# Performance work log

Hardware: AMD Instinct MI355X
Metric: run time of the kernel (lower is better)

Reference implementation:

```python
import jax, jax.numpy as jnp
import numpy as np

B, S_REF, E, H = 128, 2048, 512, 512

def setup_inputs() -> dict:
    key = jax.random.key(0)
    ks = jax.random.split(key, 13)
    def lin(kw, kb, out_d, in_d):
        bound = 1.0 / np.sqrt(in_d)
        w = jax.random.uniform(kw, (out_d, in_d), minval=-bound, maxval=bound, dtype=jnp.float32)
        b = jax.random.uniform(kb, (out_d,), minval=-bound, maxval=bound, dtype=jnp.float32)
        return w, b
    Wa_w, Wa_b = lin(ks[0], ks[1], H, H)
    Ua_w, Ua_b = lin(ks[2], ks[3], H, H)
    Va_w, Va_b = lin(ks[4], ks[5], 1, H)
    Wih_w, Wih_b = lin(ks[6], ks[7], H, E + H)
    Whh_w, Whh_b = lin(ks[8], ks[9], H, H)
    x_t = jax.random.normal(ks[10], (B, 1, E), dtype=jnp.float32)
    x_ref_encoded = jax.random.normal(ks[11], (B, S_REF, H), dtype=jnp.float32)
    h_prev = jax.random.normal(ks[12], (B, H), dtype=jnp.float32)
    return {"x_t": x_t, "x_ref_encoded": x_ref_encoded, "h_prev": h_prev,
            "Wa_w": Wa_w, "Wa_b": Wa_b, "Ua_w": Ua_w, "Ua_b": Ua_b,
            "Va_w": Va_w, "Va_b": Va_b, "Wih_w": Wih_w, "Wih_b": Wih_b,
            "Whh_w": Whh_w, "Whh_b": Whh_b}

def reference(x_t, x_ref_encoded, h_prev, Wa_w, Wa_b, Ua_w, Ua_b, Va_w, Va_b, Wih_w, Wih_b, Whh_w, Whh_b):
    # Bahdanau additive attention
    q = h_prev @ Wa_w.T + Wa_b                      # (B, H)
    k = jnp.einsum('bsh,oh->bso', x_ref_encoded, Ua_w) + Ua_b  # (B, S, H)
    scores = jnp.einsum('bsh,h->bs', jnp.tanh(q[:, None, :] + k), Va_w[0]) + Va_b[0]  # (B, S)
    attn_weights = jax.nn.softmax(scores, axis=1)
    context = jnp.einsum('bs,bsh->bh', attn_weights, x_ref_encoded)  # (B, H)
    # Reservoir RNN cell on concat(x_t[:,0,:], context)
    rnn_in = jnp.concatenate([x_t[:, 0, :], context], axis=1)        # (B, E+H)
    h_next = jnp.tanh(rnn_in @ Wih_w.T + Wih_b + h_prev @ Whh_w.T + Whh_b)
    return (h_next, context)
```

## Files before the change

kernel.cpp:

```cpp
#include <hip/hip_runtime.h>
#include <hip/hip_bf16.h>
#include <math.h>


typedef __attribute__((ext_vector_type(8))) short short8;
typedef __attribute__((ext_vector_type(8))) unsigned short ushort8;
typedef __attribute__((ext_vector_type(4))) float f32x4;

#define S_LEN 2048
#define BDIM 128
#define HDIM 512
#define EDIM 512
#define BM 64
#define NCHUNK (S_LEN / BM)

__device__ __forceinline__ unsigned short f2bf(float f) {
  unsigned int u = __float_as_uint(f);
  u += 0x7fffu + ((u >> 16) & 1u);
  return (unsigned short)(u >> 16);
}

__device__ __forceinline__ float bf2f(unsigned short u) {
  return __uint_as_float(((unsigned int)u) << 16);
}

__device__ __forceinline__ float fast_tanh(float x) {
  float e = __expf(2.0f * x);
  return 1.0f - 2.0f / (e + 1.0f);
}

__global__ __launch_bounds__(256) void k_prep(const float* __restrict__ ua_src,
                                              unsigned short* __restrict__ ua_dst,
                                              const float* __restrict__ hp,
                                              const float* __restrict__ Wa,
                                              const float* __restrict__ Wab,
                                              const float* __restrict__ Uab,
                                              float* __restrict__ q) {
  if (blockIdx.x < 128) {
    int tid = blockIdx.x * 256 + threadIdx.x;
    int ct = tid >> 10;
    int kt = (tid >> 6) & 15;
    int l = tid & 63;
    int col = ct * 16 + (l & 15);
    int k = kt * 32 + (l >> 4) * 8;
    const float4* s = (const float4*)(ua_src + (size_t)col * HDIM + k);
    float4 v0 = s[0], v1 = s[1];
    ushort8 p;
    p[0] = f2bf(v0.x); p[1] = f2bf(v0.y); p[2] = f2bf(v0.z); p[3] = f2bf(v0.w);
    p[4] = f2bf(v1.x); p[5] = f2bf(v1.y); p[6] = f2bf(v1.z); p[7] = f2bf(v1.w);
    *(ushort8*)(ua_dst + (size_t)tid * 8) = p;
  } else {
    int bq = blockIdx.x - 128;
    int b = bq >> 1, oh = bq & 1;
    int o = oh * 256 + threadIdx.x;
    __shared__ float hs[HDIM];
    hs[threadIdx.x] = hp[b * HDIM + threadIdx.x];
    hs[threadIdx.x + 256] = hp[b * HDIM + threadIdx.x + 256];
    __syncthreads();
    const float4* wr = (const float4*)(Wa + (size_t)o * HDIM);
    float acc = 0.f;
#pragma unroll 8
    for (int i = 0; i < HDIM / 4; ++i) {
      float4 v = wr[i];
      acc += v.x * hs[i * 4 + 0] + v.y * hs[i * 4 + 1] + v.z * hs[i * 4 + 2] + v.w * hs[i * 4 + 3];
    }
    q[b * HDIM + o] = acc + Wab[o] + Uab[o];
  }
}

__global__ __launch_bounds__(512, 4) void k_scores_ctx(
    const float* __restrict__ xref, const unsigned short* __restrict__ uab,
    const float* __restrict__ q, const float* __restrict__ va,
    float* __restrict__ mArr, float* __restrict__ lArr, float* __restrict__ cpart) {
  int chunk = blockIdx.x;
  int b = blockIdx.y;
  int tid = threadIdx.x;
  int l = tid & 63;
  int w = tid >> 6;
  int c = l & 15, g4 = l >> 4;

  __shared__ __align__(16) unsigned short As[BM * HDIM];
  __shared__ float sc[BM];
  __shared__ float pl[BM];

  f32x4 acc[4][4];
#pragma unroll
  for (int m = 0; m < 4; ++m)
#pragma unroll
    for (int n = 0; n < 4; ++n) acc[m][n] = f32x4{0.f, 0.f, 0.f, 0.f};

  const float* xb = xref + ((size_t)b * S_LEN + (size_t)chunk * BM) * HDIM;

  int srow = tid >> 3, skq = tid & 7;
  char* wb = (char*)&As[0] + srow * 1024 + ((skq * 16) ^ ((srow & 7) << 4));
  const float* sb = xb + (size_t)srow * HDIM + skq * 8;

  float4 a0, a1, a2, a3, a4, a5, a6, a7;
  short8 bpre[4];

#define LD2(va, vb, p)                                                         \
  {                                                                            \
    va = *(const float4*)(sb + (p) * 64);                                      \
    vb = *(const float4*)(sb + (p) * 64 + 4);                                  \
  }

#define WR1(va, vb, p)                                                         \
  {                                                                            \
    union { __hip_bfloat162 h[4]; ushort8 s; } u_;                             \
    u_.h[0] = __float22bfloat162_rn(make_float2(va.x, va.y));                  \
    u_.h[1] = __float22bfloat162_rn(make_float2(va.z, va.w));                  \
    u_.h[2] = __float22bfloat162_rn(make_float2(vb.x, vb.y));                  \
    u_.h[3] = __float22bfloat162_rn(make_float2(vb.z, vb.w));                  \
    *(ushort8*)(wb + (p) * 128) = u_.s;                                        \
  }

#define AFRAGS(kt)                                                             \
    short8 afr_[4];                                                            \
    _Pragma("unroll")                                                          \
    for (int m = 0; m < 4; ++m) {                                              \
      int row = m * 16 + (l & 15);                                             \
      int kb = ((kt) * 64 + (l >> 4) * 16) ^ ((row & 7) << 4);                 \
      afr_[m] = *(const short8*)((const char*)&As[0] + row * 1024 + kb);       \
    }

#define MFMA16(bsrc)                                                           \
    __builtin_amdgcn_s_setprio(1);                                             \
    _Pragma("unroll")                                                          \
    for (int m = 0; m < 4; ++m)                                                \
      _Pragma("unroll")                                                        \
      for (int n = 0; n < 4; ++n)                                              \
        acc[m][n] = __builtin_amdgcn_mfma_f32_16x16x32_bf16(afr_[m], bsrc[n],  \
                                                            acc[m][n], 0, 0, 0); \
    __builtin_amdgcn_s_setprio(0);

#define CLUSTER(kt)                                                            \
  {                                                                            \
    short8 bfr_[4];                                                            \
    _Pragma("unroll")                                                          \
    for (int n = 0; n < 4; ++n) {                                              \
      int ct = w * 4 + n;                                                      \
      bfr_[n] = *(const short8*)(uab + (((size_t)(ct * 16 + (kt)) * 64 + l) * 8)); \
    }                                                                          \
    AFRAGS(kt)                                                                 \
    MFMA16(bfr_)                                                               \
  }

#define CLUSTER_PRE(kt)                                                        \
  {                                                                            \
    AFRAGS(kt)                                                                 \
    MFMA16(bpre)                                                               \
  }

  LD2(a0, a1, 0) LD2(a2, a3, 1) LD2(a4, a5, 2) LD2(a6, a7, 3)
  WR1(a0, a1, 0) WR1(a2, a3, 1) WR1(a4, a5, 2) WR1(a6, a7, 3)
  LD2(a0, a1, 4) LD2(a2, a3, 5) LD2(a4, a5, 6) LD2(a6, a7, 7)
  WR1(a0, a1, 4) WR1(a2, a3, 5) WR1(a4, a5, 6) WR1(a6, a7, 7)
  if (tid < BM) sc[tid] = 0.f;
#pragma unroll
  for (int n = 0; n < 4; ++n)
    bpre[n] = *(const short8*)(uab + (((size_t)((w * 4 + n) * 16 + 0) * 64 + l) * 8));
  __syncthreads();

  CLUSTER_PRE(0)
  CLUSTER(1)  CLUSTER(2)  CLUSTER(3)
  CLUSTER(4)  CLUSTER(5)  CLUSTER(6)  CLUSTER(7)
  CLUSTER(8)  CLUSTER(9)  CLUSTER(10) CLUSTER(11)
  CLUSTER(12) CLUSTER(13)

  float qf[4], vf[4];
#pragma unroll
  for (int n = 0; n < 4; ++n) {
    int o = w * 64 + n * 16 + c;
    qf[n] = q[b * HDIM + o];
    vf[n] = va[o];
  }
  CLUSTER(14) CLUSTER(15)

#pragma unroll
  for (int m = 0; m < 4; ++m) {
#pragma unroll
    for (int r = 0; r < 4; ++r) {
      float sum = 0.f;
#pragma unroll
      for (int n = 0; n < 4; ++n) sum += fast_tanh(acc[m][n][r] + qf[n]) * vf[n];
      sum += __shfl_xor(sum, 1);
      sum += __shfl_xor(sum, 2);
      sum += __shfl_xor(sum, 4);
      sum += __shfl_xor(sum, 8);
      if (c == 0) atomicAdd(&sc[m * 16 + g4 * 4 + r], sum);
    }
  }
  __syncthreads();

  float M = sc[l];
#pragma unroll
  for (int off = 32; off >= 1; off >>= 1) M = fmaxf(M, __shfl_xor(M, off));
  float pp = __expf(sc[l] - M);
  float lsum = pp;
#pragma unroll
  for (int off = 32; off >= 1; off >>= 1) lsum += __shfl_xor(lsum, off);
  if (tid < BM) pl[tid] = pp;
  if (tid == 0) {
    mArr[b * NCHUNK + chunk] = M;
    lArr[b * NCHUNK + chunk] = lsum;
  }
  __syncthreads();

  {
    int h2 = tid * 2;
    const char* base_ = (const char*)&As[0];
    float cacc = 0.f;
#pragma unroll 8
    for (int r = 0; r < BM; ++r) {
      int byte = r * 1024 + (h2 ^ ((r & 7) << 4));
      cacc += pl[r] * bf2f(*(const unsigned short*)(base_ + byte));
    }
    cpart[((size_t)b * NCHUNK + chunk) * HDIM + tid] = cacc;
  }
#undef LD2
#undef WR1
#undef AFRAGS
#undef MFMA16
#undef CLUSTER
#undef CLUSTER_PRE
}

__global__ __launch_bounds__(512) void k_combine(const float* __restrict__ mArr,
                                                 const float* __restrict__ lArr,
                                                 const float* __restrict__ cpart,
                                                 float* __restrict__ ctx,
                                                 float* __restrict__ out_ctx) {
  int b = blockIdx.x, t = threadIdx.x;
  __shared__ float wf[NCHUNK];
  __shared__ float dinv;
  if (t == 0) {
    float M = mArr[b * NCHUNK];
    for (int i = 1; i < NCHUNK; ++i) M = fmaxf(M, mArr[b * NCHUNK + i]);
    float den = 0.f;
    for (int i = 0; i < NCHUNK; ++i) {
      float f = __expf(mArr[b * NCHUNK + i] - M);
      wf[i] = f;
      den += f * lArr[b * NCHUNK + i];
    }
    dinv = 1.0f / den;
  }
  __syncthreads();
  float s = 0.f;
#pragma unroll
  for (int i = 0; i < NCHUNK; ++i) s += wf[i] * cpart[((size_t)b * NCHUNK + i) * HDIM + t];
  float c = s * dinv;
  ctx[b * HDIM + t] = c;
  out_ctx[b * HDIM + t] = c;
}

__global__ __launch_bounds__(256) void k_rnn(const float* __restrict__ xt,
                                             const float* __restrict__ ctx,
                                             const float* __restrict__ hp,
                                             const float* __restrict__ Wih,
                                             const float* __restrict__ Wihb,
                                             const float* __restrict__ Whh,
                                             const float* __restrict__ Whhb,
                                             float* __restrict__ hout) {
  int b = blockIdx.x, oh = blockIdx.y;
  int o = oh * 256 + threadIdx.x;
  __shared__ float xs[EDIM], cs[HDIM], hs[HDIM];
  xs[threadIdx.x] = xt[b * EDIM + threadIdx.x];
  xs[threadIdx.x + 256] = xt[b * EDIM + threadIdx.x + 256];
  cs[threadIdx.x] = ctx[b * HDIM + threadIdx.x];
  cs[threadIdx.x + 256] = ctx[b * HDIM + threadIdx.x + 256];
  hs[threadIdx.x] = hp[b * HDIM + threadIdx.x];
  hs[threadIdx.x + 256] = hp[b * HDIM + threadIdx.x + 256];
  __syncthreads();
  const float4* wi = (const float4*)(Wih + (size_t)o * (EDIM + HDIM));
  float acc = Wihb[o] + Whhb[o];
#pragma unroll 8
  for (int i = 0; i < EDIM / 4; ++i) {
    float4 v = wi[i];
    acc += v.x * xs[i * 4] + v.y * xs[i * 4 + 1] + v.z * xs[i * 4 + 2] + v.w * xs[i * 4 + 3];
  }
  const float4* wi2 = wi + EDIM / 4;
#pragma unroll 8
  for (int i = 0; i < HDIM / 4; ++i) {
    float4 v = wi2[i];
    acc += v.x * cs[i * 4] + v.y * cs[i * 4 + 1] + v.z * cs[i * 4 + 2] + v.w * cs[i * 4 + 3];
  }
  const float4* wh = (const float4*)(Whh + (size_t)o * HDIM);
#pragma unroll 8
  for (int i = 0; i < HDIM / 4; ++i) {
    float4 v = wh[i];
    acc += v.x * hs[i * 4] + v.y * hs[i * 4 + 1] + v.z * hs[i * 4 + 2] + v.w * hs[i * 4 + 3];
  }
  hout[b * HDIM + o] = tanhf(acc);
}

extern "C" void kernel_launch(void* const* d_in, const int* in_sizes, int n_in,
                              void* d_out, int out_size, void* d_ws, size_t ws_size,
                              hipStream_t stream) {
  const float* x_t    = (const float*)d_in[0];
  const float* x_ref  = (const float*)d_in[1];
  const float* h_prev = (const float*)d_in[2];
  const float* Wa_w   = (const float*)d_in[3];
  const float* Wa_b   = (const float*)d_in[4];
  const float* Ua_w   = (const float*)d_in[5];
  const float* Ua_b   = (const float*)d_in[6];
  const float* Va_w   = (const float*)d_in[7];
  const float* Wih_w  = (const float*)d_in[9];
  const float* Wih_b  = (const float*)d_in[10];
  const float* Whh_w  = (const float*)d_in[11];
  const float* Whh_b  = (const float*)d_in[12];

  char* ws = (char*)d_ws;
  unsigned short* ua_fr = (unsigned short*)ws;
  float* q     = (float*)(ws + 524288);
  float* mArr  = (float*)(ws + 786432);
  float* lArr  = (float*)(ws + 802816);
  float* cpart = (float*)(ws + 819200);
  float* ctx   = (float*)(ws + 9207808);

  float* h_out   = (float*)d_out;
  float* ctx_out = h_out + BDIM * HDIM;

  k_prep<<<dim3(384), dim3(256), 0, stream>>>(Ua_w, ua_fr, h_prev, Wa_w, Wa_b, Ua_b, q);
  k_scores_ctx<<<dim3(NCHUNK, BDIM), dim3(512), 0, stream>>>(x_ref, ua_fr, q, Va_w, mArr, lArr, cpart);
  k_combine<<<dim3(BDIM), dim3(512), 0, stream>>>(mArr, lArr, cpart, ctx, ctx_out);
  k_rnn<<<dim3(BDIM, 2), dim3(256), 0, stream>>>(x_t, ctx, h_prev, Wih_w, Wih_b, Whh_w, Whh_b, h_out);
}
```

Measured before the change: 288.8 us.

## Double sequence tile to 128 rows and split output columns into two halves

Doubles the per-block sequence chunk from 64 to 128 rows, so each block loads a 128x512 bf16 tile into shared memory. The output dimension is then processed in two passes of 256 columns, each wave doing 8x2 MFMA tiles and a fused tanh/score epilogue per pass. The aim is to halve the number of chunks and the combine-stage partials, and to reuse each B fragment across more rows. In exchange, shared memory per block doubles, occupancy is capped at 2 blocks per CU, and the setprio hints are removed.

```diff
diff --git a/kernel.cpp b/kernel.cpp
--- a/kernel.cpp
+++ b/kernel.cpp
@@ -11,7 +11,7 @@
 #define BDIM 128
 #define HDIM 512
 #define EDIM 512
-#define BM 64
+#define BM 128
 #define NCHUNK (S_LEN / BM)
 
 __device__ __forceinline__ unsigned short f2bf(float f) {
@@ -68,7 +68,7 @@
   }
 }
 
-__global__ __launch_bounds__(512, 4) void k_scores_ctx(
+__global__ __launch_bounds__(512, 2) void k_scores_ctx(
     const float* __restrict__ xref, const unsigned short* __restrict__ uab,
     const float* __restrict__ q, const float* __restrict__ va,
     float* __restrict__ mArr, float* __restrict__ lArr, float* __restrict__ cpart) {
@@ -83,62 +83,63 @@
   __shared__ float sc[BM];
   __shared__ float pl[BM];
 
-  f32x4 acc[4][4];
-#pragma unroll
-  for (int m = 0; m < 4; ++m)
-#pragma unroll
-    for (int n = 0; n < 4; ++n) acc[m][n] = f32x4{0.f, 0.f, 0.f, 0.f};
+  f32x4 acc[8][2];
+#pragma unroll
+  for (int m = 0; m < 8; ++m)
+#pragma unroll
+    for (int n = 0; n < 2; ++n) acc[m][n] = f32x4{0.f, 0.f, 0.f, 0.f};
 
   const float* xb = xref + ((size_t)b * S_LEN + (size_t)chunk * BM) * HDIM;
 
   int srow = tid >> 3, skq = tid & 7;
-  char* wb = (char*)&As[0] + srow * 1024 + ((skq * 16) ^ ((srow & 7) << 4));
-  const float* sb = xb + (size_t)srow * HDIM + skq * 8;
+  int swo = (skq * 16) ^ ((srow & 7) << 4);
+  char* wb0 = (char*)&As[0] + srow * 1024 + swo;
+  char* wb1 = (char*)&As[0] + (srow + 64) * 1024 + swo;
+  const float* sb0 = xb + (size_t)srow * HDIM + skq * 8;
+  const float* sb1 = sb0 + (size_t)64 * HDIM;
 
   float4 a0, a1, a2, a3, a4, a5, a6, a7;
-  short8 bpre[4];
-
-#define LD2(va, vb, p)                                                         \
-  {                                                                            \
-    va = *(const float4*)(sb + (p) * 64);                                      \
-    vb = *(const float4*)(sb + (p) * 64 + 4);                                  \
-  }
-
-#define WR1(va, vb, p)                                                         \
+  short8 bpre[2];
+
+#define LD2(va, vb, sb, p)                                                     \
+  {                                                                            \
+    va = *(const float4*)((sb) + (p) * 64);                                    \
+    vb = *(const float4*)((sb) + (p) * 64 + 4);                                \
+  }
+
+#define WR1(va, vb, wb, p)                                                     \
   {                                                                            \
     union { __hip_bfloat162 h[4]; ushort8 s; } u_;                             \
     u_.h[0] = __float22bfloat162_rn(make_float2(va.x, va.y));                  \
     u_.h[1] = __float22bfloat162_rn(make_float2(va.z, va.w));                  \
     u_.h[2] = __float22bfloat162_rn(make_float2(vb.x, vb.y));                  \
     u_.h[3] = __float22bfloat162_rn(make_float2(vb.z, vb.w));                  \
-    *(ushort8*)(wb + (p) * 128) = u_.s;                                        \
+    *(ushort8*)((wb) + (p) * 128) = u_.s;                                      \
   }
 
 #define AFRAGS(kt)                                                             \
-    short8 afr_[4];                                                            \
+    short8 afr_[8];                                                            \
     _Pragma("unroll")                                                          \
-    for (int m = 0; m < 4; ++m) {                                              \
+    for (int m = 0; m < 8; ++m) {                                              \
       int row = m * 16 + (l & 15);                                             \
       int kb = ((kt) * 64 + (l >> 4) * 16) ^ ((row & 7) << 4);                 \
       afr_[m] = *(const short8*)((const char*)&As[0] + row * 1024 + kb);       \
     }
 
 #define MFMA16(bsrc)                                                           \
-    __builtin_amdgcn_s_setprio(1);                                             \
     _Pragma("unroll")                                                          \
-    for (int m = 0; m < 4; ++m)                                                \
+    for (int m = 0; m < 8; ++m)                                                \
       _Pragma("unroll")                                                        \
-      for (int n = 0; n < 4; ++n)                                              \
+      for (int n = 0; n < 2; ++n)                                              \
         acc[m][n] = __builtin_amdgcn_mfma_f32_16x16x32_bf16(afr_[m], bsrc[n],  \
-                                                            acc[m][n], 0, 0, 0); \
-    __builtin_amdgcn_s_setprio(0);
-
-#define CLUSTER(kt)                                                            \
-  {                                                                            \
-    short8 bfr_[4];                                                            \
+                                                            acc[m][n], 0, 0, 0);
+
+#define CLUSTER(h, kt)                                                         \
+  {                                                                            \
+    short8 bfr_[2];                                                            \
     _Pragma("unroll")                                                          \
-    for (int n = 0; n < 4; ++n) {                                              \
-      int ct = w * 4 + n;                                                      \
+    for (int n = 0; n < 2; ++n) {                                              \
+      int ct = (h) * 16 + w * 2 + n;                                           \
       bfr_[n] = *(const short8*)(uab + (((size_t)(ct * 16 + (kt)) * 64 + l) * 8)); \
     }                                                                          \
     AFRAGS(kt)                                                                 \
@@ -151,55 +152,71 @@
     MFMA16(bpre)                                                               \
   }
 
-  LD2(a0, a1, 0) LD2(a2, a3, 1) LD2(a4, a5, 2) LD2(a6, a7, 3)
-  WR1(a0, a1, 0) WR1(a2, a3, 1) WR1(a4, a5, 2) WR1(a6, a7, 3)
-  LD2(a0, a1, 4) LD2(a2, a3, 5) LD2(a4, a5, 6) LD2(a6, a7, 7)
-  WR1(a0, a1, 4) WR1(a2, a3, 5) WR1(a4, a5, 6) WR1(a6, a7, 7)
+#define EPI(h)                                                                 \
+  {                                                                            \
+    float qf0, qf1, vf0, vf1;                                                  \
+    {                                                                          \
+      int o0 = (h) * 256 + w * 32 + c, o1 = o0 + 16;                           \
+      qf0 = q[b * HDIM + o0]; qf1 = q[b * HDIM + o1];                          \
+      vf0 = va[o0]; vf1 = va[o1];                                              \
+    }                                                                          \
+    _Pragma("unroll")                                                          \
+    for (int m = 0; m < 8; ++m) {                                              \
+      _Pragma("unroll")                                                        \
+      for (int r = 0; r < 4; ++r) {                                            \
+        float sum = fast_tanh(acc[m][0][r] + qf0) * vf0 +                      \
+                    fast_tanh(acc[m][1][r] + qf1) * vf1;                       \
+        sum += __shfl_xor(sum, 1);                                             \
+        sum += __shfl_xor(sum, 2);                                             \
+        sum += __shfl_xor(sum, 4);                                             \
+        sum += __shfl_xor(sum, 8);                                             \
+        if (c == 0) atomicAdd(&sc[m * 16 + g4 * 4 + r], sum);                  \
+      }                                                                        \
+    }                                                                          \
+  }
+
+  LD2(a0, a1, sb0, 0) LD2(a2, a3, sb0, 1) LD2(a4, a5, sb0, 2) LD2(a6, a7, sb0, 3)
+  WR1(a0, a1, wb0, 0) WR1(a2, a3, wb0, 1) WR1(a4, a5, wb0, 2) WR1(a6, a7, wb0, 3)
+  LD2(a0, a1, sb0, 4) LD2(a2, a3, sb0, 5) LD2(a4, a5, sb0, 6) LD2(a6, a7, sb0, 7)
+  WR1(a0, a1, wb0, 4) WR1(a2, a3, wb0, 5) WR1(a4, a5, wb0, 6) WR1(a6, a7, wb0, 7)
+  LD2(a0, a1, sb1, 0) LD2(a2, a3, sb1, 1) LD2(a4, a5, sb1, 2) LD2(a6, a7, sb1, 3)
+  WR1(a0, a1, wb1, 0) WR1(a2, a3, wb1, 1) WR1(a4, a5, wb1, 2) WR1(a6, a7, wb1, 3)
+  LD2(a0, a1, sb1, 4) LD2(a2, a3, sb1, 5) LD2(a4, a5, sb1, 6) LD2(a6, a7, sb1, 7)
+  WR1(a0, a1, wb1, 4) WR1(a2, a3, wb1, 5) WR1(a4, a5, wb1, 6) WR1(a6, a7, wb1, 7)
   if (tid < BM) sc[tid] = 0.f;
 #pragma unroll
-  for (int n = 0; n < 4; ++n)
-    bpre[n] = *(const short8*)(uab + (((size_t)((w * 4 + n) * 16 + 0) * 64 + l) * 8));
+  for (int n = 0; n < 2; ++n)
+    bpre[n] = *(const short8*)(uab + (((size_t)((w * 2 + n) * 16 + 0) * 64 + l) * 8));
   __syncthreads();
 
   CLUSTER_PRE(0)
-  CLUSTER(1)  CLUSTER(2)  CLUSTER(3)
-  CLUSTER(4)  CLUSTER(5)  CLUSTER(6)  CLUSTER(7)
-  CLUSTER(8)  CLUSTER(9)  CLUSTER(10) CLUSTER(11)
-  CLUSTER(12) CLUSTER(13)
-
-  float qf[4], vf[4];
-#pragma unroll
-  for (int n = 0; n < 4; ++n) {
-    int o = w * 64 + n * 16 + c;
-    qf[n] = q[b * HDIM + o];
-    vf[n] = va[o];
-  }
-  CLUSTER(14) CLUSTER(15)
-
-#pragma unroll
-  for (int m = 0; m < 4; ++m) {
-#pragma unroll
-    for (int r = 0; r < 4; ++r) {
-      float sum = 0.f;
-#pragma unroll
-      for (int n = 0; n < 4; ++n) sum += fast_tanh(acc[m][n][r] + qf[n]) * vf[n];
-      sum += __shfl_xor(sum, 1);
-      sum += __shfl_xor(sum, 2);
-      sum += __shfl_xor(sum, 4);
-      sum += __shfl_xor(sum, 8);
-      if (c == 0) atomicAdd(&sc[m * 16 + g4 * 4 + r], sum);
-    }
-  }
-  __syncthreads();
-
-  float M = sc[l];
+  CLUSTER(0, 1)  CLUSTER(0, 2)  CLUSTER(0, 3)
+  CLUSTER(0, 4)  CLUSTER(0, 5)  CLUSTER(0, 6)  CLUSTER(0, 7)
+  CLUSTER(0, 8)  CLUSTER(0, 9)  CLUSTER(0, 10) CLUSTER(0, 11)
+  CLUSTER(0, 12) CLUSTER(0, 13) CLUSTER(0, 14) CLUSTER(0, 15)
+  EPI(0)
+
+#pragma unroll
+  for (int m = 0; m < 8; ++m)
+#pragma unroll
+    for (int n = 0; n < 2; ++n) acc[m][n] = f32x4{0.f, 0.f, 0.f, 0.f};
+
+  CLUSTER(1, 0)  CLUSTER(1, 1)  CLUSTER(1, 2)  CLUSTER(1, 3)
+  CLUSTER(1, 4)  CLUSTER(1, 5)  CLUSTER(1, 6)  CLUSTER(1, 7)
+  CLUSTER(1, 8)  CLUSTER(1, 9)  CLUSTER(1, 10) CLUSTER(1, 11)
+  CLUSTER(1, 12) CLUSTER(1, 13) CLUSTER(1, 14) CLUSTER(1, 15)
+  EPI(1)
+  __syncthreads();
+
+  float s0 = sc[l], s1 = sc[l + 64];
+  float M = fmaxf(s0, s1);
 #pragma unroll
   for (int off = 32; off >= 1; off >>= 1) M = fmaxf(M, __shfl_xor(M, off));
-  float pp = __expf(sc[l] - M);
-  float lsum = pp;
+  float p0 = __expf(s0 - M), p1 = __expf(s1 - M);
+  float lsum = p0 + p1;
 #pragma unroll
   for (int off = 32; off >= 1; off >>= 1) lsum += __shfl_xor(lsum, off);
-  if (tid < BM) pl[tid] = pp;
+  if (w == 0) { pl[l] = p0; pl[l + 64] = p1; }
   if (tid == 0) {
     mArr[b * NCHUNK + chunk] = M;
     lArr[b * NCHUNK + chunk] = lsum;
@@ -223,6 +240,7 @@
 #undef MFMA16
 #undef CLUSTER
 #undef CLUSTER_PRE
+#undef EPI
 }
 
 __global__ __launch_bounds__(512) void k_combine(const float* __restrict__ mArr,
```

After: 378.5 us. +31.1%, slower.
